# Performance work log

Hardware: AMD Instinct MI355X
Metric: run time of the kernel (lower is better)

The kernel has to match this reference:

```python
import jax, jax.numpy as jnp
import numpy as np

EPS = 1e-6
QMAX = 127.0  # hif8 emulated as symmetric 8-bit fake-quant (true hif8 numerics are proprietary)


def _rotate_half(v):
    d = v.shape[-1] // 2
    return jnp.concatenate([-v[..., d:], v[..., :d]], axis=-1)


def _quant(v):
    # per-row (last-axis) absmax quantization emulating hif8 with a per-tensor-row scale
    amax = jnp.max(jnp.abs(v), axis=-1, keepdims=True)
    scale = jnp.maximum(amax / QMAX, 1e-8)
    q = jnp.round(v / scale)
    return q, jnp.squeeze(scale, -1)


def setup_inputs() -> dict:
    key = jax.random.key(0)
    ks = jax.random.split(key, 16)
    B, S, H, Hn, D, L = 2, 4096, 2048, 32, 128, 16384
    return {
        "x": jax.random.normal(ks[0], (B, S, H), jnp.float32),
        "q_norm": jax.random.uniform(ks[1], (H,), jnp.float32),
        "q_norm_scale": jax.random.uniform(ks[2], (H,), jnp.float32),
        "w_qb": jax.random.normal(ks[3], (H, Hn * D), jnp.float32),
        "w_qb_scale": jax.random.uniform(ks[4], (Hn * D,), jnp.float32),
        "wk": jax.random.normal(ks[5], (H, D), jnp.float32),
        "w_proj": jax.random.normal(ks[6], (H, Hn), jnp.float32),
        "ln_gamma_k": jax.random.uniform(ks[7], (H,), jnp.float32),
        "ln_beta_k": jax.random.normal(ks[8], (H,), jnp.float32),
        "cos_idx_rope": jax.random.uniform(ks[9], (S, D), jnp.float32),
        "sin_idx_rope": jax.random.uniform(ks[10], (S, D), jnp.float32),
        "hadamard_q": jax.random.normal(ks[11], (D, D), jnp.float32),
        "hadamard_k": jax.random.normal(ks[12], (D, D), jnp.float32),
        "k_cache": jnp.zeros((L, D), jnp.float32),
        "k_cache_scale": jnp.zeros((L,), jnp.float32),
        "k_cache_index": jnp.arange(B * S, dtype=jnp.int32).reshape(B, S),
    }


def reference(x, q_norm, q_norm_scale, w_qb, w_qb_scale, wk, w_proj,
              ln_gamma_k, ln_beta_k, cos_idx_rope, sin_idx_rope,
              hadamard_q, hadamard_k, k_cache, k_cache_scale, k_cache_index):
    B, S, H = x.shape
    D = hadamard_q.shape[0]
    Hn = w_qb.shape[1] // D

    # ---- Q branch: RMSNorm + smooth scale -> quantized GEMM (dequant fused) ----
    rms = jax.lax.rsqrt(jnp.mean(x * x, axis=-1, keepdims=True) + EPS)
    xq = x * rms * q_norm * q_norm_scale                      # [B,S,H]
    q = jnp.einsum('bsh,hd->bsd', xq, w_qb) * w_qb_scale      # [B,S,Hn*D]
    q = q.reshape(B, S, Hn, D)

    cos_q = cos_idx_rope[:S][None, :, None, :]
    sin_q = sin_idx_rope[:S][None, :, None, :]
    q = q * cos_q + _rotate_half(q) * sin_q                   # RoPE
    q = jnp.einsum('bshd,de->bshe', q, hadamard_q)            # Hadamard mix
    q_hif8, q_scale = _quant(q)                               # [B,S,Hn,D], [B,S,Hn]

    # ---- K branch: LayerNorm -> proj -> RoPE -> Hadamard -> quant ----
    mu = jnp.mean(x, axis=-1, keepdims=True)
    var = jnp.mean(jnp.square(x - mu), axis=-1, keepdims=True)
    xk = (x - mu) * jax.lax.rsqrt(var + EPS) * ln_gamma_k + ln_beta_k
    k = jnp.einsum('bsh,hd->bsd', xk, wk)                     # [B,S,D]
    cos_k = cos_idx_rope[:S][None, :, :]
    sin_k = sin_idx_rope[:S][None, :, :]
    k = k * cos_k + _rotate_half(k) * sin_k
    k = jnp.einsum('bsd,de->bse', k, hadamard_k)
    k_q, k_s = _quant(k)                                      # [B,S,D], [B,S]

    # ---- scatter quantized K into the indexer cache ----
    idx = k_cache_index.reshape(-1)
    k_hif8 = k_cache.at[idx].set(k_q.reshape(-1, D))
    k_scale = k_cache_scale.at[idx].set(k_s.reshape(-1))

    # ---- per-head indexer weights ----
    weights = jnp.einsum('bsh,he->bse', x, w_proj)            # [B,S,Hn]

    return (q_hif8, q_scale, k_hif8, k_scale, weights)
```

## Files before the change

### kernel.cpp

```cpp
#include <hip/hip_runtime.h>
#include <hip/hip_bf16.h>
#include <stdint.h>

constexpr int Mrows = 8192;
constexpr int Hdim  = 2048;
constexpr int Sdim  = 4096;
constexpr int HnD   = 4096;
constexpr int Hn    = 32;
constexpr int Dd    = 128;
constexpr int Lc    = 16384;
constexpr int NFULL = 4352;

typedef unsigned short u16;
typedef __attribute__((ext_vector_type(8))) short    bf16x8;
typedef __attribute__((ext_vector_type(4))) float    f32x4;
typedef __attribute__((ext_vector_type(8))) unsigned short u16x8;

__device__ __forceinline__ u16 f2bf(float f) {
    union { float f; unsigned int i; } v; v.f = f;
    unsigned int x = v.i;
    return (u16)((x + 0x7fffu + ((x >> 16) & 1u)) >> 16);
}
__device__ __forceinline__ void gload_lds16(const void* g, void* l) {
    __builtin_amdgcn_global_load_lds(
        (const __attribute__((address_space(1))) void*)g,
        (__attribute__((address_space(3))) void*)l, 16, 0, 0);
}

__global__ __launch_bounds__(256) void fused_prep(
    const float* __restrict__ x, u16* __restrict__ xb, float* __restrict__ rms,
    float* __restrict__ mu, float* __restrict__ rstd,
    const float* __restrict__ wqb, const float* __restrict__ qn, const float* __restrict__ qns,
    const float* __restrict__ wk,  const float* __restrict__ g,  const float* __restrict__ wproj,
    u16* __restrict__ wt,
    const float* __restrict__ hq, const float* __restrict__ hk,
    u16* __restrict__ hqt, u16* __restrict__ hkt,
    const float* __restrict__ b,
    float* __restrict__ bdot, float* __restrict__ gdot,
    const float* __restrict__ kc, const float* __restrict__ kcs,
    float* __restrict__ dk, float* __restrict__ dks)
{
    __shared__ u16 utile[64 * 72];
    __shared__ float sred[8];
    int bid = blockIdx.x, t = threadIdx.x;

    if (bid < 8192) {
        int r = bid;
        const float4* xr = (const float4*)(x + (size_t)r * Hdim);
        float4 a4 = xr[2 * t], b4 = xr[2 * t + 1];
        float v[8] = {a4.x, a4.y, a4.z, a4.w, b4.x, b4.y, b4.z, b4.w};
        float s = 0.f, ss = 0.f;
        __align__(16) u16 o[8];
        #pragma unroll
        for (int i = 0; i < 8; i++) { s += v[i]; ss += v[i] * v[i]; o[i] = f2bf(v[i]); }
        ((u16x8*)(xb + (size_t)r * Hdim))[t] = *(const u16x8*)o;
        for (int oo = 32; oo > 0; oo >>= 1) { s += __shfl_down(s, oo); ss += __shfl_down(ss, oo); }
        if ((t & 63) == 0) { sred[t >> 6] = s; sred[4 + (t >> 6)] = ss; }
        __syncthreads();
        if (t == 0) {
            float S1 = sred[0] + sred[1] + sred[2] + sred[3];
            float S2 = sred[4] + sred[5] + sred[6] + sred[7];
            float mean = S1 / Hdim, msq = S2 / Hdim;
            rms[r]  = rsqrtf(msq + 1e-6f);
            mu[r]   = mean;
            rstd[r] = rsqrtf(msq - mean * mean + 1e-6f);
        }
    } else if (bid < 10368) {
        int b2 = bid - 8192;
        int k0 = (b2 & 31) * 64, n0 = (b2 >> 5) * 64;
        int lk = t >> 2, lc0 = (t & 3) * 16;
        int k = k0 + lk;
        float c1k = qn[k] * qns[k];
        float gk  = g[k];
        #pragma unroll
        for (int i = 0; i < 16; i++) {
            int n = n0 + lc0 + i;
            float val;
            if (n < 4096)      val = wqb[(size_t)k * HnD + n] * c1k;
            else if (n < 4224) val = wk[k * Dd + (n - 4096)] * gk;
            else if (n < 4256) val = wproj[k * Hn + (n - 4224)];
            else               val = 0.f;
            utile[lk * 72 + lc0 + i] = f2bf(val);
        }
        __syncthreads();
        int ln = t >> 2, lk0 = (t & 3) * 16;
        __align__(16) u16 o[16];
        #pragma unroll
        for (int i = 0; i < 16; i++) o[i] = utile[(lk0 + i) * 72 + ln];
        u16* dst = wt + (size_t)(n0 + ln) * Hdim + k0 + lk0;
        *(u16x8*)dst = *(const u16x8*)o;
        *(u16x8*)(dst + 8) = *((const u16x8*)o + 1);
    } else if (bid < 10376) {
        int q = bid - 10368;
        int matq = q >> 2, tr = (q >> 1) & 1, tc = q & 1;
        const float* src = matq ? hk : hq;
        u16* dst = matq ? hkt : hqt;
        int r = t >> 2, c0 = (t & 3) * 16;
        #pragma unroll
        for (int i = 0; i < 4; i++) {
            float4 vv = *(const float4*)(src + (size_t)(tr * 64 + r) * Dd + tc * 64 + c0 + 4 * i);
            utile[r * 72 + c0 + 4 * i]     = f2bf(vv.x);
            utile[r * 72 + c0 + 4 * i + 1] = f2bf(vv.y);
            utile[r * 72 + c0 + 4 * i + 2] = f2bf(vv.z);
            utile[r * 72 + c0 + 4 * i + 3] = f2bf(vv.w);
        }
        __syncthreads();
        int n = t >> 2, k0 = (t & 3) * 16;
        __align__(16) u16 o[16];
        #pragma unroll
        for (int i = 0; i < 16; i++) o[i] = utile[(k0 + i) * 72 + n];
        u16* dp = dst + (size_t)(tc * 64 + n) * Dd + tr * 64 + k0;
        *(u16x8*)dp = *(const u16x8*)o;
        *(u16x8*)(dp + 8) = *((const u16x8*)o + 1);
    } else if (bid < 10504) {
        int n = bid - 10376;
        float sb = 0.f, sg = 0.f;
        for (int k = t; k < Hdim; k += 256) {
            float w = wk[k * Dd + n];
            sb += b[k] * w;
            sg += g[k] * w;
        }
        for (int o = 32; o > 0; o >>= 1) { sb += __shfl_down(sb, o); sg += __shfl_down(sg, o); }
        if ((t & 63) == 0) { sred[t >> 6] = sb; sred[4 + (t >> 6)] = sg; }
        __syncthreads();
        if (t == 0) {
            bdot[n] = sred[0] + sred[1] + sred[2] + sred[3];
            gdot[n] = sred[4] + sred[5] + sred[6] + sred[7];
        }
    } else {
        int gg = (bid - 10504) * 256 + t;
        ((float4*)dk)[2 * gg]     = ((const float4*)kc)[2 * gg];
        ((float4*)dk)[2 * gg + 1] = ((const float4*)kc)[2 * gg + 1];
        if (gg < Lc / 8) {
            ((float4*)dks)[2 * gg]     = ((const float4*)kcs)[2 * gg];
            ((float4*)dks)[2 * gg + 1] = ((const float4*)kcs)[2 * gg + 1];
        }
    }
}

#define RA(bufo, ks, mt) (*(const bf16x8*)(lds + (bufo) * 65536 + (ks) * 16384 + \
    (wr * 64 + (mt) * 16 + l15) * 64 + rsw))
#define RB(bufo, ks, nh, j) (*(const bf16x8*)(lds + (bufo) * 65536 + 32768 + (ks) * 16384 + \
    (wc * 128 + (nh) * 64 + (j) * 16 + l15) * 64 + rsw))
#define SA(tt, ks) do { \
    const u16* gp_ = Ab + (size_t)srow * Hdim + (tt) * 64 + (ks) * 32 + scol; \
    char* dp_ = lds + (((tt) & 1) * 65536) + (ks) * 16384 + wq; \
    gload_lds16(gp_, dp_); \
    gload_lds16(gp_ + (size_t)128 * Hdim, dp_ + 8192); \
} while (0)
#define SB(tt, ks) do { \
    const u16* gp_ = Bb + (size_t)srow * Hdim + (tt) * 64 + (ks) * 32 + scol; \
    char* dp_ = lds + (((tt) & 1) * 65536) + 32768 + (ks) * 16384 + wq; \
    gload_lds16(gp_, dp_); \
    gload_lds16(gp_ + (size_t)128 * Hdim, dp_ + 8192); \
} while (0)
#define VM6 do { asm volatile("s_waitcnt vmcnt(6)" ::: "memory"); __builtin_amdgcn_sched_barrier(0); } while (0)
#define VM0 do { asm volatile("s_waitcnt vmcnt(0)" ::: "memory"); __builtin_amdgcn_sched_barrier(0); } while (0)
#define NOPS ((void)0)
#define PH(bufo, ks, nh, STG, WT) do { \
    if ((nh) == 0) { \
        _Pragma("unroll") for (int mt = 0; mt < 4; mt++) af[mt] = RA(bufo, ks, mt); \
    } \
    _Pragma("unroll") for (int j = 0; j < 4; j++) bfr[j] = RB(bufo, ks, nh, j); \
    STG; \
    asm volatile("s_waitcnt lgkmcnt(0)" ::: "memory"); \
    __builtin_amdgcn_sched_barrier(0); \
    __builtin_amdgcn_s_setprio(1); \
    _Pragma("unroll") for (int mt = 0; mt < 4; mt++) \
        _Pragma("unroll") for (int j = 0; j < 4; j++) \
            acc[mt][(nh) * 4 + j] = __builtin_amdgcn_mfma_f32_16x16x32_bf16( \
                af[mt], bfr[j], acc[mt][(nh) * 4 + j], 0, 0, 0); \
    __builtin_amdgcn_s_setprio(0); \
    WT; \
    __builtin_amdgcn_s_barrier(); \
} while (0)

__global__ __launch_bounds__(512, 1) void main_gemm(
    const u16* __restrict__ A, const u16* __restrict__ Bt,
    const float* __restrict__ rms, const float* __restrict__ qbs,
    const u16* __restrict__ hqt,
    const float* __restrict__ cosr, const float* __restrict__ sinr,
    float* __restrict__ oq, float* __restrict__ oqs)
{
    __shared__ __align__(16) char lds[131072];

    int tid = threadIdx.x;
    int w = tid >> 6, lane = tid & 63, quad = lane >> 4, l15 = lane & 15;
    int wr = w & 3, wc = w >> 2;
    int bm = blockIdx.x, bn = blockIdx.y;
    int brow = bm * 256;
    int rsw = (quad ^ ((l15 >> 1) & 3)) * 16;

    const u16* Ab = A  + (size_t)brow * Hdim;
    const u16* Bb = Bt + (size_t)(bn * 256) * Hdim;

    int srow = tid >> 2;
    int scol = (((tid & 3) ^ ((srow >> 1) & 3)) * 8);
    int wq = w * 1024;

    bf16x8 af[4], bfr[4];
    f32x4 acc[4][8] = {};

    SA(0, 0); SB(0, 0); SA(0, 1); SB(0, 1); SA(1, 0); SB(1, 0); SA(1, 1);
    VM6;
    __builtin_amdgcn_s_barrier();

    for (int I = 0; I < 15; I++) {
        int t1 = 2 * I + 1, t2 = 2 * I + 2, t3 = 2 * I + 3;
        PH(0, 0, 0, SB(t1, 1), NOPS);
        PH(0, 0, 1, SA(t2, 0), NOPS);
        PH(0, 1, 0, SB(t2, 0), NOPS);
        PH(0, 1, 1, SA(t2, 1), VM6);
        PH(1, 0, 0, SB(t2, 1), NOPS);
        PH(1, 0, 1, SA(t3, 0), NOPS);
        PH(1, 1, 0, SB(t3, 0), NOPS);
        PH(1, 1, 1, SA(t3, 1), VM6);
    }
    PH(0, 0, 0, SB(31, 1), NOPS);
    PH(0, 0, 1, NOPS, NOPS);
    PH(0, 1, 0, NOPS, NOPS);
    PH(0, 1, 1, NOPS, VM0);
    PH(1, 0, 0, NOPS, NOPS);
    PH(1, 0, 1, NOPS, NOPS);
    PH(1, 1, 0, NOPS, NOPS);
    PH(1, 1, 1, NOPS, NOPS);

    __syncthreads();
    int head = bn * 2 + wc;
    char* Pw = lds + w * 16384;
    float qb[8];
    #pragma unroll
    for (int nt = 0; nt < 8; nt++) qb[nt] = qbs[head * 128 + nt * 16 + l15];
    #pragma unroll
    for (int mt = 0; mt < 4; mt++) {
        float y[8][4];
        #pragma unroll
        for (int reg = 0; reg < 4; reg++) {
            float rv = rms[brow + wr * 64 + mt * 16 + quad * 4 + reg];
            #pragma unroll
            for (int nt = 0; nt < 8; nt++) y[nt][reg] = acc[mt][nt][reg] * rv * qb[nt];
        }
        #pragma unroll
        for (int reg = 0; reg < 4; reg++) {
            int rp = mt * 16 + quad * 4 + reg;
            int s_ = (brow + wr * 64 + rp) & (Sdim - 1);
            const float* cr = cosr + (size_t)s_ * Dd + l15;
            const float* sr = sinr + (size_t)s_ * Dd + l15;
            int sw = (rp & 7) << 4;
            #pragma unroll
            for (int nt = 0; nt < 8; nt++) {
                float c  = cr[nt * 16];
                float sv = sr[nt * 16];
                float sign = (nt < 4) ? -1.f : 1.f;
                float o = y[nt][reg] * c + sign * y[nt ^ 4][reg] * sv;
                int colb = (nt * 16 + l15) * 2;
                *(u16*)(Pw + rp * 256 + (colb ^ sw)) = f2bf(o);
            }
        }
    }
    __syncthreads();
    #pragma unroll
    for (int mt = 0; mt < 4; mt++) {
        bf16x8 pa[4];
        #pragma unroll
        for (int kb = 0; kb < 4; kb++) {
            int row = mt * 16 + l15;
            pa[kb] = *(const bf16x8*)(Pw + row * 256 + ((kb * 64 + quad * 16) ^ ((row & 7) << 4)));
        }
        f32x4 a2[8] = {};
        #pragma unroll
        for (int nt = 0; nt < 8; nt++) {
            #pragma unroll
            for (int kb = 0; kb < 4; kb++) {
                bf16x8 hb = *(const bf16x8*)(hqt + (size_t)(nt * 16 + l15) * Dd + kb * 32 + quad * 8);
                a2[nt] = __builtin_amdgcn_mfma_f32_16x16x32_bf16(pa[kb], hb, a2[nt], 0, 0, 0);
            }
        }
        #pragma unroll
        for (int reg = 0; reg < 4; reg++) {
            float m = 0.f;
            #pragma unroll
            for (int nt = 0; nt < 8; nt++) m = fmaxf(m, fabsf(a2[nt][reg]));
            m = fmaxf(m, __shfl_xor(m, 8));
            m = fmaxf(m, __shfl_xor(m, 4));
            m = fmaxf(m, __shfl_xor(m, 2));
            m = fmaxf(m, __shfl_xor(m, 1));
            float scale = fmaxf(m * (1.f / 127.f), 1e-8f);
            float inv = 1.f / scale;
            int r = brow + wr * 64 + mt * 16 + quad * 4 + reg;
            float* orow = oq + (size_t)r * HnD + head * 128;
            #pragma unroll
            for (int nt = 0; nt < 8; nt++)
                orow[nt * 16 + l15] = rintf(a2[nt][reg] * inv);
            if (l15 == 0) oqs[(size_t)r * Hn + head] = scale;
        }
    }
}

__global__ __launch_bounds__(256) void k_branch(
    const u16* __restrict__ A, const u16* __restrict__ Bt,
    const float* __restrict__ rstd, const float* __restrict__ mu,
    const float* __restrict__ bdot, const float* __restrict__ gdot,
    const u16* __restrict__ hkt,
    const float* __restrict__ cosr, const float* __restrict__ sinr,
    const int* __restrict__ idx,
    float* __restrict__ ok, float* __restrict__ oks, float* __restrict__ wout)
{
    __shared__ __align__(16) char klds[73728];
    __shared__ float pamax[32][2];
    __shared__ int sidx[32];
    int tid = threadIdx.x, w = tid >> 6, lane = tid & 63, quad = lane >> 4, l15 = lane & 15;
    int blk = blockIdx.x;
    int mh = w & 1, ngrp = w >> 1;
    const u16* Ab = A + (size_t)(blk * 32) * Hdim;
    const u16* Bb = Bt + (size_t)4096 * Hdim;
    int F[5];
    F[0] = ngrp * 2; F[1] = ngrp * 2 + 1; F[2] = 4 + ngrp * 2; F[3] = 5 + ngrp * 2; F[4] = 8 + ngrp;
    int ar = tid >> 3, ach = ((tid & 7) ^ (ar & 7)) * 8;
    int wq1 = w * 1024;

#define KSTG(slotn, st) do { \
    gload_lds16(Ab + (size_t)ar * Hdim + (st) * 64 + ach, klds + (slotn) * 24576 + wq1); \
    _Pragma("unroll") for (int u = 0; u < 5; u++) { \
        int ix = u * 256 + tid; int br = ix >> 3; int bch = ((ix & 7) ^ (br & 7)) * 8; \
        gload_lds16(Bb + (size_t)br * Hdim + (st) * 64 + bch, \
                    klds + (slotn) * 24576 + 4096 + u * 4096 + wq1); \
    } \
} while (0)
#define KRA(slotn, ks) (*(const bf16x8*)(klds + (slotn) * 24576 + \
    (mh * 16 + l15) * 128 + ((((ks) * 4 + quad) ^ (l15 & 7)) * 16)))
#define KRB(slotn, ks, f) (*(const bf16x8*)(klds + (slotn) * 24576 + 4096 + \
    ((f) * 16 + l15) * 128 + ((((ks) * 4 + quad) ^ (l15 & 7)) * 16)))

    f32x4 acc[5] = {};
    KSTG(0, 0); KSTG(1, 1);
    asm volatile("s_waitcnt vmcnt(6)" ::: "memory");
    __builtin_amdgcn_sched_barrier(0);
    __builtin_amdgcn_s_barrier();
    int sl = 0;
    for (int s = 0; s < 32; s++) {
        bf16x8 ka[2], kbf[2][5];
        ka[0] = KRA(sl, 0); ka[1] = KRA(sl, 1);
        #pragma unroll
        for (int j = 0; j < 5; j++) { kbf[0][j] = KRB(sl, 0, F[j]); kbf[1][j] = KRB(sl, 1, F[j]); }
        if (s + 2 < 32) { int ns = sl + 2; if (ns >= 3) ns -= 3; KSTG(ns, s + 2); }
        asm volatile("s_waitcnt lgkmcnt(0)" ::: "memory");
        __builtin_amdgcn_sched_barrier(0);
        __builtin_amdgcn_s_setprio(1);
        #pragma unroll
        for (int ks = 0; ks < 2; ks++)
            #pragma unroll
            for (int j = 0; j < 5; j++)
                acc[j] = __builtin_amdgcn_mfma_f32_16x16x32_bf16(ka[ks], kbf[ks][j], acc[j], 0, 0, 0);
        __builtin_amdgcn_s_setprio(0);
        if (s < 30) { asm volatile("s_waitcnt vmcnt(6)" ::: "memory"); }
        else        { asm volatile("s_waitcnt vmcnt(0)" ::: "memory"); }
        __builtin_amdgcn_sched_barrier(0);
        __builtin_amdgcn_s_barrier();
        sl++; if (sl == 3) sl = 0;
    }

    if (tid < 32) sidx[tid] = idx[blk * 32 + tid];
    __syncthreads();
    u16* sP = (u16*)klds;
    #pragma unroll
    for (int reg = 0; reg < 4; reg++) {
        int rl = mh * 16 + quad * 4 + reg;
        int r = blk * 32 + rl;
        float sd = rstd[r], m_ = mu[r];
        int s_ = r & (Sdim - 1);
        float v[4];
        #pragma unroll
        for (int j = 0; j < 4; j++) {
            int col = F[j] * 16 + l15;
            v[j] = acc[j][reg] * sd + bdot[col] - sd * m_ * gdot[col];
        }
        #pragma unroll
        for (int j = 0; j < 4; j++) {
            int col = F[j] * 16 + l15;
            float c = cosr[(size_t)s_ * Dd + col], sv = sinr[(size_t)s_ * Dd + col];
            float sign = (j < 2) ? -1.f : 1.f;
            sP[rl * 136 + col] = f2bf(v[j] * c + sign * v[j ^ 2] * sv);
        }
        wout[(size_t)r * Hn + (F[4] - 8) * 16 + l15] = acc[4][reg];
    }
    __syncthreads();
    f32x4 a2[4] = {};
    #pragma unroll
    for (int kb4 = 0; kb4 < 4; kb4++) {
        bf16x8 pa = *(const bf16x8*)(sP + (mh * 16 + l15) * 136 + kb4 * 32 + quad * 8);
        #pragma unroll
        for (int nt = 0; nt < 4; nt++) {
            bf16x8 hb = *(const bf16x8*)(hkt + (size_t)(ngrp * 64 + nt * 16 + l15) * Dd + kb4 * 32 + quad * 8);
            a2[nt] = __builtin_amdgcn_mfma_f32_16x16x32_bf16(pa, hb, a2[nt], 0, 0, 0);
        }
    }
    #pragma unroll
    for (int reg = 0; reg < 4; reg++) {
        float m = 0.f;
        #pragma unroll
        for (int nt = 0; nt < 4; nt++) m = fmaxf(m, fabsf(a2[nt][reg]));
        m = fmaxf(m, __shfl_xor(m, 8));
        m = fmaxf(m, __shfl_xor(m, 4));
        m = fmaxf(m, __shfl_xor(m, 2));
        m = fmaxf(m, __shfl_xor(m, 1));
        if (l15 == 0) pamax[mh * 16 + quad * 4 + reg][ngrp] = m;
    }
    __syncthreads();
    #pragma unroll
    for (int reg = 0; reg < 4; reg++) {
        int rl = mh * 16 + quad * 4 + reg;
        float am = fmaxf(pamax[rl][0], pamax[rl][1]);
        float scale = fmaxf(am * (1.f / 127.f), 1e-8f);
        float inv = 1.f / scale;
        size_t dro = (size_t)sidx[rl] * Dd;
        #pragma unroll
        for (int nt = 0; nt < 4; nt++)
            ok[dro + ngrp * 64 + nt * 16 + l15] = rintf(a2[nt][reg] * inv);
        if (l15 == 0 && ngrp == 0) oks[sidx[rl]] = scale;
    }
}

extern "C" void kernel_launch(void* const* d_in, const int* in_sizes, int n_in,
                              void* d_out, int out_size, void* d_ws, size_t ws_size,
                              hipStream_t stream) {
    (void)in_sizes; (void)n_in; (void)out_size; (void)ws_size;
    const float* x    = (const float*)d_in[0];
    const float* qn   = (const float*)d_in[1];
    const float* qns  = (const float*)d_in[2];
    const float* wqb  = (const float*)d_in[3];
    const float* wqbs = (const float*)d_in[4];
    const float* wk   = (const float*)d_in[5];
    const float* wpj  = (const float*)d_in[6];
    const float* g    = (const float*)d_in[7];
    const float* b    = (const float*)d_in[8];
    const float* cosr = (const float*)d_in[9];
    const float* sinr = (const float*)d_in[10];
    const float* hq   = (const float*)d_in[11];
    const float* hk   = (const float*)d_in[12];
    const float* kc   = (const float*)d_in[13];
    const float* kcs  = (const float*)d_in[14];
    const int*   idx  = (const int*)d_in[15];

    char* ws = (char*)d_ws;
    size_t o = 0;
    u16* xb  = (u16*)(ws + o); o += (size_t)Mrows * Hdim * 2;
    u16* wt  = (u16*)(ws + o); o += (size_t)NFULL * Hdim * 2;
    u16* hqt = (u16*)(ws + o); o += Dd * Dd * 2;
    u16* hkt = (u16*)(ws + o); o += Dd * Dd * 2;
    float* rmsb  = (float*)(ws + o); o += (size_t)Mrows * 4;
    float* mub   = (float*)(ws + o); o += (size_t)Mrows * 4;
    float* rstdb = (float*)(ws + o); o += (size_t)Mrows * 4;
    float* bdotb = (float*)(ws + o); o += 512;
    float* gdotb = (float*)(ws + o); o += 512;

    float* out = (float*)d_out;
    float* oq  = out;
    float* oqs = oq  + (size_t)Mrows * HnD;
    float* ok  = oqs + (size_t)Mrows * Hn;
    float* oks = ok  + (size_t)Lc * Dd;
    float* ow  = oks + Lc;

    fused_prep<<<11528, 256, 0, stream>>>(
        x, xb, rmsb, mub, rstdb, wqb, qn, qns, wk, g, wpj, wt,
        hq, hk, hqt, hkt, b, bdotb, gdotb, kc, kcs, ok, oks);
    main_gemm<<<dim3(Mrows / 256, 16), 512, 0, stream>>>(
        xb, wt, rmsb, wqbs, hqt, cosr, sinr, oq, oqs);
    k_branch<<<Mrows / 32, 256, 0, stream>>>(
        xb, wt, rstdb, mub, bdotb, gdotb, hkt, cosr, sinr, idx, ok, oks, ow);
}
```

Measured before the change: 457.9 us.

## Restructure main GEMM pipeline into four full-width phases and relax scheduling barriers

```diff
diff --git a/kernel.cpp b/kernel.cpp
--- a/kernel.cpp
+++ b/kernel.cpp
@@ -140,8 +140,8 @@
 
 #define RA(bufo, ks, mt) (*(const bf16x8*)(lds + (bufo) * 65536 + (ks) * 16384 + \
     (wr * 64 + (mt) * 16 + l15) * 64 + rsw))
-#define RB(bufo, ks, nh, j) (*(const bf16x8*)(lds + (bufo) * 65536 + 32768 + (ks) * 16384 + \
-    (wc * 128 + (nh) * 64 + (j) * 16 + l15) * 64 + rsw))
+#define RB(bufo, ks, j) (*(const bf16x8*)(lds + (bufo) * 65536 + 32768 + (ks) * 16384 + \
+    (wc * 128 + (j) * 16 + l15) * 64 + rsw))
 #define SA(tt, ks) do { \
     const u16* gp_ = Ab + (size_t)srow * Hdim + (tt) * 64 + (ks) * 32 + scol; \
     char* dp_ = lds + (((tt) & 1) * 65536) + (ks) * 16384 + wq; \
@@ -154,22 +154,20 @@
     gload_lds16(gp_, dp_); \
     gload_lds16(gp_ + (size_t)128 * Hdim, dp_ + 8192); \
 } while (0)
-#define VM6 do { asm volatile("s_waitcnt vmcnt(6)" ::: "memory"); __builtin_amdgcn_sched_barrier(0); } while (0)
-#define VM0 do { asm volatile("s_waitcnt vmcnt(0)" ::: "memory"); __builtin_amdgcn_sched_barrier(0); } while (0)
+#define VM8 asm volatile("s_waitcnt vmcnt(8)" ::: "memory")
+#define VM4 asm volatile("s_waitcnt vmcnt(4)" ::: "memory")
+#define VM0 asm volatile("s_waitcnt vmcnt(0)" ::: "memory")
 #define NOPS ((void)0)
-#define PH(bufo, ks, nh, STG, WT) do { \
-    if ((nh) == 0) { \
-        _Pragma("unroll") for (int mt = 0; mt < 4; mt++) af[mt] = RA(bufo, ks, mt); \
-    } \
-    _Pragma("unroll") for (int j = 0; j < 4; j++) bfr[j] = RB(bufo, ks, nh, j); \
+#define PH2(bufo, ks, STG, WT) do { \
+    bf16x8 af[4], bq[8]; \
+    _Pragma("unroll") for (int mt = 0; mt < 4; mt++) af[mt] = RA(bufo, ks, mt); \
+    _Pragma("unroll") for (int j = 0; j < 8; j++) bq[j] = RB(bufo, ks, j); \
     STG; \
-    asm volatile("s_waitcnt lgkmcnt(0)" ::: "memory"); \
-    __builtin_amdgcn_sched_barrier(0); \
     __builtin_amdgcn_s_setprio(1); \
     _Pragma("unroll") for (int mt = 0; mt < 4; mt++) \
-        _Pragma("unroll") for (int j = 0; j < 4; j++) \
-            acc[mt][(nh) * 4 + j] = __builtin_amdgcn_mfma_f32_16x16x32_bf16( \
-                af[mt], bfr[j], acc[mt][(nh) * 4 + j], 0, 0, 0); \
+        _Pragma("unroll") for (int j = 0; j < 8; j++) \
+            acc[mt][j] = __builtin_amdgcn_mfma_f32_16x16x32_bf16( \
+                af[mt], bq[j], acc[mt][j], 0, 0, 0); \
     __builtin_amdgcn_s_setprio(0); \
     WT; \
     __builtin_amdgcn_s_barrier(); \
@@ -198,32 +196,24 @@
     int scol = (((tid & 3) ^ ((srow >> 1) & 3)) * 8);
     int wq = w * 1024;
 
-    bf16x8 af[4], bfr[4];
     f32x4 acc[4][8] = {};
 
-    SA(0, 0); SB(0, 0); SA(0, 1); SB(0, 1); SA(1, 0); SB(1, 0); SA(1, 1);
-    VM6;
+    SA(0, 0); SB(0, 0); SA(0, 1); SB(0, 1); SA(1, 0); SB(1, 0);
+    VM8;
     __builtin_amdgcn_s_barrier();
 
+    #pragma unroll 1
     for (int I = 0; I < 15; I++) {
-        int t1 = 2 * I + 1, t2 = 2 * I + 2, t3 = 2 * I + 3;
-        PH(0, 0, 0, SB(t1, 1), NOPS);
-        PH(0, 0, 1, SA(t2, 0), NOPS);
-        PH(0, 1, 0, SB(t2, 0), NOPS);
-        PH(0, 1, 1, SA(t2, 1), VM6);
-        PH(1, 0, 0, SB(t2, 1), NOPS);
-        PH(1, 0, 1, SA(t3, 0), NOPS);
-        PH(1, 1, 0, SB(t3, 0), NOPS);
-        PH(1, 1, 1, SA(t3, 1), VM6);
-    }
-    PH(0, 0, 0, SB(31, 1), NOPS);
-    PH(0, 0, 1, NOPS, NOPS);
-    PH(0, 1, 0, NOPS, NOPS);
-    PH(0, 1, 1, NOPS, VM0);
-    PH(1, 0, 0, NOPS, NOPS);
-    PH(1, 0, 1, NOPS, NOPS);
-    PH(1, 1, 0, NOPS, NOPS);
-    PH(1, 1, 1, NOPS, NOPS);
+        int t0 = 2 * I, t1 = 2 * I + 1;
+        PH2(0, 0, SA(t0 + 1, 1); SB(t0 + 1, 1), VM8);
+        PH2(0, 1, SA(t0 + 2, 0); SB(t0 + 2, 0), VM8);
+        PH2(1, 0, SA(t1 + 1, 1); SB(t1 + 1, 1), VM8);
+        PH2(1, 1, SA(t1 + 2, 0); SB(t1 + 2, 0), VM8);
+    }
+    PH2(0, 0, SA(31, 1); SB(31, 1), VM8);
+    PH2(0, 1, NOPS, VM4);
+    PH2(1, 0, NOPS, VM0);
+    PH2(1, 1, NOPS, NOPS);
 
     __syncthreads();
     int head = bn * 2 + wc;
@@ -335,7 +325,6 @@
     f32x4 acc[5] = {};
     KSTG(0, 0); KSTG(1, 1);
     asm volatile("s_waitcnt vmcnt(6)" ::: "memory");
-    __builtin_amdgcn_sched_barrier(0);
     __builtin_amdgcn_s_barrier();
     int sl = 0;
     for (int s = 0; s < 32; s++) {
@@ -344,8 +333,6 @@
         #pragma unroll
         for (int j = 0; j < 5; j++) { kbf[0][j] = KRB(sl, 0, F[j]); kbf[1][j] = KRB(sl, 1, F[j]); }
         if (s + 2 < 32) { int ns = sl + 2; if (ns >= 3) ns -= 3; KSTG(ns, s + 2); }
-        asm volatile("s_waitcnt lgkmcnt(0)" ::: "memory");
-        __builtin_amdgcn_sched_barrier(0);
         __builtin_amdgcn_s_setprio(1);
         #pragma unroll
         for (int ks = 0; ks < 2; ks++)
@@ -355,7 +342,6 @@
         __builtin_amdgcn_s_setprio(0);
         if (s < 30) { asm volatile("s_waitcnt vmcnt(6)" ::: "memory"); }
         else        { asm volatile("s_waitcnt vmcnt(0)" ::: "memory"); }
-        __builtin_amdgcn_sched_barrier(0);
         __builtin_amdgcn_s_barrier();
         sl++; if (sl == 3) sl = 0;
     }
```

Result: no change. 453.0 us (-1.1%).
